# Performance work log

Hardware: AMD Instinct MI355X
Metric: run time of the kernel (lower is better)

Reference implementation:

```python
import jax, jax.numpy as jnp
import numpy as np
from jax import lax

DIM = 192
HEADS = 8


def conv3d(x, w, b, groups=1, pad=0):
    # x: [B,C,T,H,W], w: [O, C//groups, kt, kh, kw]
    out = lax.conv_general_dilated(
        x, w, window_strides=(1, 1, 1),
        padding=[(pad, pad)] * 3,
        dimension_numbers=('NCDHW', 'OIDHW', 'NCDHW'),
        feature_group_count=groups)
    return out + b[None, :, None, None, None]


def setup_inputs() -> dict:
    key = jax.random.key(0)
    ks = jax.random.split(key, 8)
    d = DIM
    x = jax.random.normal(ks[0], (2, d, 8, 64, 64), dtype=jnp.float32)
    qkv_w = jax.random.normal(ks[1], (3 * d, d, 1, 1, 1), dtype=jnp.float32) * 0.02
    qkv_b = jnp.zeros((3 * d,), dtype=jnp.float32)
    dw_w = jax.random.normal(ks[2], (3 * d, 1, 3, 3, 3), dtype=jnp.float32) * 0.02
    dw_b = jnp.zeros((3 * d,), dtype=jnp.float32)
    temperature = jnp.ones((HEADS, 1, 1), dtype=jnp.float32)
    proj_w = jax.random.normal(ks[3], (d, d, 1, 1, 1), dtype=jnp.float32) * 0.02
    proj_b = jnp.zeros((d,), dtype=jnp.float32)
    return {"x": x, "qkv_w": qkv_w, "qkv_b": qkv_b, "dw_w": dw_w,
            "dw_b": dw_b, "temperature": temperature,
            "proj_w": proj_w, "proj_b": proj_b}


def reference(x, qkv_w, qkv_b, dw_w, dw_b, temperature, proj_w, proj_b):
    b, c, t, h, w = x.shape
    head_dim = c // HEADS
    n = t * h * w
    qkv = conv3d(x, qkv_w, qkv_b)                      # [b, 3c, t, h, w]
    qkv = conv3d(qkv, dw_w, dw_b, groups=3 * c, pad=1)  # depthwise 3x3x3
    q, k, v = jnp.split(qkv, 3, axis=1)
    def to_heads(z):
        return z.reshape(b, HEADS, head_dim, n)         # b head c (thw)
    q, k, v = to_heads(q), to_heads(k), to_heads(v)
    # L2 normalize along token axis (F.normalize, eps=1e-12)
    q = q / jnp.maximum(jnp.linalg.norm(q, axis=-1, keepdims=True), 1e-12)
    k = k / jnp.maximum(jnp.linalg.norm(k, axis=-1, keepdims=True), 1e-12)
    attn = jnp.einsum('bhcn,bhdn->bhcd', q, k) * temperature  # [b,H,hd,hd]
    attn = jax.nn.softmax(attn, axis=-1)
    out = jnp.einsum('bhcd,bhdn->bhcn', attn, v)        # [b,H,hd,n]
    out = out.reshape(b, c, t, h, w)
    return conv3d(out, proj_w, proj_b)
```

## Files before the change

kernel.cpp:

```cpp
#include <hip/hip_runtime.h>

#define NTOK 32768
#define CIN 192
#define C3 576
#define HEADS 8
#define HD 24

typedef __attribute__((ext_vector_type(8))) short bf16x8;
typedef __attribute__((ext_vector_type(16))) float f32x16;
typedef __attribute__((ext_vector_type(4))) unsigned int u32x4;

__device__ __forceinline__ float bf2f(unsigned int u) {
  union { unsigned int i; float f; } x; x.i = u << 16; return x.f;
}
__device__ __forceinline__ unsigned short f2bf(float f) {
  union { float f; unsigned int i; } x; x.f = f;
  unsigned int r = x.i + 0x7fffu + ((x.i >> 16) & 1u);
  return (unsigned short)(r >> 16);
}

__global__ __launch_bounds__(256) void k_wfrag(const float* __restrict__ W,
                                               unsigned short* __restrict__ Wf,
                                               int nchunk) {
  const int g = blockIdx.x * 256 + threadIdx.x;
  if (g >= nchunk) return;
  const int ol = g & 63, hi = (g >> 6) & 1, kk = (g >> 7) % 12, ot = g / 1536;
  const float* src = W + (size_t)(ot * 64 + ol) * CIN + kk * 16 + hi * 8;
  bf16x8 p;
#pragma unroll
  for (int e = 0; e < 8; ++e) p[e] = (short)f2bf(src[e]);
  *(bf16x8*)&Wf[(size_t)g * 8] = p;
}

template<int XBF, int OUTF32>
__global__ __launch_bounds__(256, 2) void k_gemm_rr(
    const void* __restrict__ Xv, const unsigned short* __restrict__ Wf0,
    const float* __restrict__ bias, void* __restrict__ Yv, int ot_per,
    long xbs, long ybs, long wbs)
{
  __shared__ __align__(16) unsigned short Xl[192][68];
  const int tid = threadIdx.x;
  const int b = blockIdx.z;
  const int n0 = blockIdx.x * 64;
  const unsigned short* Wf = Wf0 + (size_t)b * wbs;

  if (XBF) {
    const unsigned short* X = (const unsigned short*)Xv + (size_t)b * xbs;
#pragma unroll
    for (int i = 0; i < 12; ++i) {
      const int g = tid + i * 256;
      const int c = g >> 4, nq = (g & 15) * 4;
      *(unsigned long long*)&Xl[c][nq] =
          *(const unsigned long long*)&X[(size_t)c * NTOK + n0 + nq];
    }
  } else {
    const float* X = (const float*)Xv + (size_t)b * xbs;
#pragma unroll
    for (int i = 0; i < 12; ++i) {
      const int g = tid + i * 256;
      const int c = g >> 4, nq = (g & 15) * 4;
      float4 v = *(const float4*)&X[(size_t)c * NTOK + n0 + nq];
      unsigned short p[4] = {f2bf(v.x), f2bf(v.y), f2bf(v.z), f2bf(v.w)};
      *(unsigned long long*)&Xl[c][nq] = *(unsigned long long*)p;
    }
  }
  __syncthreads();

  const int lane = tid & 63;
  const int wv = tid >> 6;
  const int o_w = (wv >> 1) * 32;
  const int n_w = (wv & 1) * 32;
  const int j = lane & 31;
  const int hi = lane >> 5;

  bf16x8 bfr[12];
#pragma unroll
  for (int kk = 0; kk < 12; ++kk)
#pragma unroll
    for (int e = 0; e < 8; ++e)
      bfr[kk][e] = (short)Xl[kk * 16 + hi * 8 + e][n_w + j];

  for (int it = 0; it < ot_per; ++it) {
    const int o0 = it * 64;
    const unsigned short* wp =
        Wf + ((size_t)it * 1536 + hi * 64 + o_w + j) * 8;

    bf16x8 a[12];
#pragma unroll
    for (int kk = 0; kk < 12; ++kk) {
      unsigned long long ad = (unsigned long long)(wp + kk * 1024);
      asm volatile("global_load_dwordx4 %0, %1, off"
                   : "=v"(a[kk]) : "v"(ad));
    }
    asm volatile("s_waitcnt vmcnt(0)" ::: "memory");
    __builtin_amdgcn_sched_barrier(0);

    f32x16 acc0, acc1;
#pragma unroll
    for (int i = 0; i < 16; ++i) { acc0[i] = 0.f; acc1[i] = 0.f; }
#pragma unroll
    for (int kp = 0; kp < 6; ++kp) {
      acc0 = __builtin_amdgcn_mfma_f32_32x32x16_bf16(a[2 * kp], bfr[2 * kp], acc0, 0, 0, 0);
      acc1 = __builtin_amdgcn_mfma_f32_32x32x16_bf16(a[2 * kp + 1], bfr[2 * kp + 1], acc1, 0, 0, 0);
    }

    if (OUTF32) {
      float* Y = (float*)Yv + (size_t)b * ybs;
#pragma unroll
      for (int r = 0; r < 16; ++r) {
        const int row = o_w + (r & 3) + 8 * (r >> 2) + 4 * hi;
        Y[(size_t)(o0 + row) * NTOK + n0 + n_w + j] =
            acc0[r] + acc1[r] + bias[o0 + row];
      }
    } else {
      unsigned short* Y = (unsigned short*)Yv + (size_t)b * ybs;
#pragma unroll
      for (int r = 0; r < 16; ++r) {
        const int row = o_w + (r & 3) + 8 * (r >> 2) + 4 * hi;
        Y[(size_t)(o0 + row) * NTOK + n0 + n_w + j] =
            f2bf(acc0[r] + acc1[r] + bias[o0 + row]);
      }
    }
  }
}

__global__ __launch_bounds__(256, 4) void k_dwconv(
    const unsigned short* __restrict__ in0,
    const float* __restrict__ wdw,
    const float* __restrict__ bdw,
    unsigned short* __restrict__ out0)
{
  __shared__ __align__(16) unsigned short s[8][18][76];
  const int tid = threadIdx.x;
  const int ch = blockIdx.y;
  const int h0 = blockIdx.x * 16;
  const size_t boff = (size_t)blockIdx.z * C3 * NTOK;
  const unsigned short* inch = in0 + boff + (size_t)ch * NTOK;

  for (int r = tid; r < 144; r += 256) {
    const int t = r / 18, rr = r % 18;
    s[t][rr][7] = 0;
    s[t][rr][72] = 0;
  }
  for (int idx = tid; idx < 144 * 8; idx += 256) {
    const int row = idx >> 3, seg = idx & 7;
    const int t = row / 18, rr = row % 18;
    const int h = h0 + rr - 1;
    u32x4 v = {0u, 0u, 0u, 0u};
    if (h >= 0 && h < 64)
      v = *(const u32x4*)&inch[t * 4096 + h * 64 + seg * 8];
    *(u32x4*)&s[t][rr][8 + seg * 8] = v;
  }
  float wr[27];
#pragma unroll
  for (int i = 0; i < 27; ++i) wr[i] = wdw[ch * 27 + i];
  const float bias = bdw[ch];
  __syncthreads();

  const int wloc = tid & 63;
  const int hl0 = (tid >> 6) * 4;
  float acc[8][4];
#pragma unroll
  for (int t = 0; t < 8; ++t)
#pragma unroll
    for (int i = 0; i < 4; ++i) acc[t][i] = 0.f;

#pragma unroll
  for (int tt = 0; tt < 8; ++tt) {
    float v[6][3];
#pragma unroll
    for (int r = 0; r < 6; ++r)
#pragma unroll
      for (int c = 0; c < 3; ++c)
        v[r][c] = bf2f(s[tt][hl0 + r][7 + wloc + c]);
#pragma unroll
    for (int p = 0; p < 3; ++p) {
      const int t = tt + 1 - p;
      if (t < 0 || t > 7) continue;
#pragma unroll
      for (int hi = 0; hi < 4; ++hi) {
        float a = 0.f;
#pragma unroll
        for (int dh = 0; dh < 3; ++dh)
#pragma unroll
          for (int dw = 0; dw < 3; ++dw)
            a += wr[p * 9 + dh * 3 + dw] * v[hi + dh][dw];
        acc[t][hi] += a;
      }
    }
  }

  unsigned short* outch = out0 + boff + (size_t)ch * NTOK;
#pragma unroll
  for (int t = 0; t < 8; ++t)
#pragma unroll
    for (int hi = 0; hi < 4; ++hi)
      outch[t * 4096 + (h0 + hl0 + hi) * 64 + wloc] = f2bf(acc[t][hi] + bias);
}

__global__ __launch_bounds__(256) void k_gram(
    const unsigned short* __restrict__ post0, float* __restrict__ Sp0)
{
  const int tid = threadIdx.x;
  const int h = blockIdx.y;
  const unsigned short* post = post0 + (size_t)blockIdx.z * C3 * NTOK;
  float* Sp = Sp0 + (size_t)blockIdx.z * HEADS * 32 * 640;
  const int lane = tid & 63;
  const int wv = tid >> 6;
  const int c = lane & 31;
  const int off = (lane >> 5) * 8;
  const unsigned short* q = post + (size_t)(h * HD + c) * NTOK;
  const unsigned short* k = post + (size_t)(192 + h * HD + c) * NTOK;

  __shared__ float Sl[24][25];
  __shared__ float nl[48];
  for (int i = tid; i < 600; i += 256) ((float*)Sl)[i] = 0.f;
  if (tid < 48) nl[tid] = 0.f;
  __syncthreads();

  f32x16 acc;
#pragma unroll
  for (int i = 0; i < 16; ++i) acc[i] = 0.f;
  float sqq = 0.f, sqk = 0.f;

  const int base = blockIdx.x * 1024 + wv * 256 + off;
#pragma unroll
  for (int i = 0; i < 16; ++i) {
    const int n = base + i * 16;
    bf16x8 a = *(const bf16x8*)&q[n];
    bf16x8 b = *(const bf16x8*)&k[n];
#pragma unroll
    for (int e = 0; e < 8; ++e) {
      float fa = bf2f((unsigned short)a[e]);
      float fb = bf2f((unsigned short)b[e]);
      sqq += fa * fa;
      sqk += fb * fb;
    }
    acc = __builtin_amdgcn_mfma_f32_32x32x16_bf16(a, b, acc, 0, 0, 0);
  }

  sqq += __shfl_down(sqq, 32, 64);
  sqk += __shfl_down(sqk, 32, 64);
  if (lane < 32 && c < 24) {
    atomicAdd(&nl[c], sqq);
    atomicAdd(&nl[24 + c], sqk);
  }
  if (c < 24) {
#pragma unroll
    for (int r = 0; r < 16; ++r) {
      const int row = (r & 3) + 8 * (r >> 2) + 4 * (lane >> 5);
      if (row < 24) atomicAdd(&Sl[row][c], acc[r]);
    }
  }
  __syncthreads();
  float* outp = Sp + ((size_t)h * 32 + blockIdx.x) * 640;
  for (int i = tid; i < 576; i += 256) outp[i] = Sl[i / 24][i % 24];
  if (tid < 48) outp[576 + tid] = nl[tid];
}

__global__ __launch_bounds__(256) void k_attn_wfrag(
    const float* __restrict__ Sp0, const float* __restrict__ temp,
    const float* __restrict__ projw, unsigned short* __restrict__ wfc0)
{
  const int h = blockIdx.x;
  const int tid = threadIdx.x;
  const float* base = Sp0 + (size_t)blockIdx.y * HEADS * 32 * 640 +
                      (size_t)h * 32 * 640;
  unsigned short* wfc = wfc0 + (size_t)blockIdx.y * 3 * 1536 * 8;

  __shared__ float Ssum[24][25];
  __shared__ float attn[24][25];
  __shared__ float nqs[24], nks[24];

  for (int i = tid; i < 576; i += 256) {
    float a = 0.f;
#pragma unroll 4
    for (int ch = 0; ch < 32; ++ch) a += base[(size_t)ch * 640 + i];
    Ssum[i / 24][i % 24] = a;
  }
  if (tid < 48) {
    float a = 0.f;
#pragma unroll 4
    for (int ch = 0; ch < 32; ++ch) a += base[(size_t)ch * 640 + 576 + tid];
    float nv = fmaxf(sqrtf(a), 1e-12f);
    if (tid < 24) nqs[tid] = nv; else nks[tid - 24] = nv;
  }
  __syncthreads();
  if (tid < 24) {
    const int c = tid;
    const float tmp = temp[h];
    float row[24];
    float m = -1e30f;
#pragma unroll
    for (int d = 0; d < 24; ++d) {
      float v = Ssum[c][d] / (nqs[c] * nks[d]) * tmp;
      row[d] = v;
      m = fmaxf(m, v);
    }
    float ssum = 0.f;
#pragma unroll
    for (int d = 0; d < 24; ++d) { float e = __expf(row[d] - m); row[d] = e; ssum += e; }
    const float inv = 1.f / ssum;
#pragma unroll
    for (int d = 0; d < 24; ++d) attn[c][d] = row[d] * inv;
  }
  __syncthreads();
  for (int e = tid; e < 192 * 24; e += 256) {
    const int o = e / 24, d = e % 24;
    float a = 0.f;
#pragma unroll
    for (int c = 0; c < 24; ++c) a += projw[o * 192 + h * 24 + c] * attn[c][d];
    const int c2 = h * 24 + d;
    const int ot = o >> 6, ol = o & 63;
    const int kk = c2 >> 4, hi = (c2 >> 3) & 1, e2 = c2 & 7;
    wfc[(size_t)((((ot * 12 + kk) * 2 + hi) * 64) + ol) * 8 + e2] = f2bf(a);
  }
}

extern "C" void kernel_launch(void* const* d_in, const int* in_sizes, int n_in,
                              void* d_out, int out_size, void* d_ws, size_t ws_size,
                              hipStream_t stream) {
  const float* x      = (const float*)d_in[0];
  const float* qkv_w  = (const float*)d_in[1];
  const float* qkv_b  = (const float*)d_in[2];
  const float* dw_w   = (const float*)d_in[3];
  const float* dw_b   = (const float*)d_in[4];
  const float* temp   = (const float*)d_in[5];
  const float* proj_w = (const float*)d_in[6];
  const float* proj_b = (const float*)d_in[7];
  float* out = (float*)d_out;

  char* ws = (char*)d_ws;
  size_t off = 0;
  unsigned short* post = (unsigned short*)(ws + off);
  off += (size_t)2 * C3 * NTOK * sizeof(unsigned short);
  unsigned short* pre = (unsigned short*)(ws + off);
  off += (size_t)2 * C3 * NTOK * sizeof(unsigned short);
  float* Sp = (float*)(ws + off);
  off += (size_t)2 * HEADS * 32 * 640 * sizeof(float);
  off = (off + 255) & ~(size_t)255;
  unsigned short* wfq = (unsigned short*)(ws + off);
  off += (size_t)9 * 1536 * 8 * sizeof(unsigned short);
  unsigned short* wfc = (unsigned short*)(ws + off);
  off += (size_t)2 * 3 * 1536 * 8 * sizeof(unsigned short);

  k_wfrag<<<54, 256, 0, stream>>>(qkv_w, wfq, 9 * 1536);

  k_gemm_rr<0, 0><<<dim3(512, 1, 2), 256, 0, stream>>>(
      x, wfq, qkv_b, pre, 9, (long)CIN * NTOK, (long)C3 * NTOK, 0);

  k_dwconv<<<dim3(4, C3, 2), 256, 0, stream>>>(pre, dw_w, dw_b, post);

  k_gram<<<dim3(32, HEADS, 2), 256, 0, stream>>>(post, Sp);

  k_attn_wfrag<<<dim3(HEADS, 2), 256, 0, stream>>>(Sp, temp, proj_w, wfc);

  k_gemm_rr<1, 1><<<dim3(512, 1, 2), 256, 0, stream>>>(
      post + (size_t)384 * NTOK, wfc, proj_b, out, 3,
      (long)C3 * NTOK, (long)CIN * NTOK, (long)3 * 1536 * 8);
}
```

Measured before the change: 146.2 us.

## Split GEMM output tiles across grid y and double-buffer weight fragment loads

The 1x1x1 conv GEMMs now spread output-channel tiles over a second grid dimension (3 chunks), so each block handles 3 or 1 tiles instead of 9 or 3. This raises parallelism, at the cost of each block reloading and re-converting its X tile into LDS. For the QKV GEMM, the weight fragment loads for the next tile are issued before the current tile's MFMAs, using partial vmcnt waits to overlap global loads with compute. The output projection uses one tile per block with no prefetch.

New measurement: 156.0 us. +6.7%, slower.

```diff
diff --git a/kernel.cpp b/kernel.cpp
--- a/kernel.cpp
+++ b/kernel.cpp
@@ -32,15 +32,25 @@
   *(bf16x8*)&Wf[(size_t)g * 8] = p;
 }
 
-template<int XBF, int OUTF32>
+__device__ __forceinline__ void issue12(bf16x8 (&a)[12],
+                                        const unsigned short* p) {
+#pragma unroll
+  for (int kk = 0; kk < 12; ++kk) {
+    unsigned long long ad = (unsigned long long)(p + kk * 1024);
+    asm volatile("global_load_dwordx4 %0, %1, off" : "=v"(a[kk]) : "v"(ad));
+  }
+}
+
+template<int XBF, int OUTF32, int OT>
 __global__ __launch_bounds__(256, 2) void k_gemm_rr(
     const void* __restrict__ Xv, const unsigned short* __restrict__ Wf0,
-    const float* __restrict__ bias, void* __restrict__ Yv, int ot_per,
+    const float* __restrict__ bias, void* __restrict__ Yv,
     long xbs, long ybs, long wbs)
 {
   __shared__ __align__(16) unsigned short Xl[192][68];
   const int tid = threadIdx.x;
   const int b = blockIdx.z;
+  const int oc = blockIdx.y;
   const int n0 = blockIdx.x * 64;
   const unsigned short* Wf = Wf0 + (size_t)b * wbs;
 
@@ -80,21 +90,11 @@
     for (int e = 0; e < 8; ++e)
       bfr[kk][e] = (short)Xl[kk * 16 + hi * 8 + e][n_w + j];
 
-  for (int it = 0; it < ot_per; ++it) {
-    const int o0 = it * 64;
-    const unsigned short* wp =
-        Wf + ((size_t)it * 1536 + hi * 64 + o_w + j) * 8;
-
-    bf16x8 a[12];
-#pragma unroll
-    for (int kk = 0; kk < 12; ++kk) {
-      unsigned long long ad = (unsigned long long)(wp + kk * 1024);
-      asm volatile("global_load_dwordx4 %0, %1, off"
-                   : "=v"(a[kk]) : "v"(ad));
-    }
-    asm volatile("s_waitcnt vmcnt(0)" ::: "memory");
-    __builtin_amdgcn_sched_barrier(0);
-
+  const int ob = oc * OT * 64;
+  const unsigned short* wbase =
+      Wf + ((size_t)(oc * OT) * 1536 + hi * 64 + o_w + j) * 8;
+
+  auto tile = [&](bf16x8 (&a)[12], int o0) {
     f32x16 acc0, acc1;
 #pragma unroll
     for (int i = 0; i < 16; ++i) { acc0[i] = 0.f; acc1[i] = 0.f; }
@@ -103,7 +103,6 @@
       acc0 = __builtin_amdgcn_mfma_f32_32x32x16_bf16(a[2 * kp], bfr[2 * kp], acc0, 0, 0, 0);
       acc1 = __builtin_amdgcn_mfma_f32_32x32x16_bf16(a[2 * kp + 1], bfr[2 * kp + 1], acc1, 0, 0, 0);
     }
-
     if (OUTF32) {
       float* Y = (float*)Yv + (size_t)b * ybs;
 #pragma unroll
@@ -121,6 +120,27 @@
             f2bf(acc0[r] + acc1[r] + bias[o0 + row]);
       }
     }
+  };
+
+  bf16x8 aA[12], aB[12];
+  if (OT == 1) {
+    issue12(aA, wbase);
+    asm volatile("s_waitcnt vmcnt(0)" ::: "memory");
+    __builtin_amdgcn_sched_barrier(0);
+    tile(aA, ob);
+  } else {
+    issue12(aA, wbase);
+    asm volatile("s_waitcnt vmcnt(0)" ::: "memory");
+    __builtin_amdgcn_sched_barrier(0);
+    issue12(aB, wbase + 12288);
+    tile(aA, ob);
+    asm volatile("s_waitcnt vmcnt(16)" ::: "memory");
+    __builtin_amdgcn_sched_barrier(0);
+    issue12(aA, wbase + 24576);
+    tile(aB, ob + 64);
+    asm volatile("s_waitcnt vmcnt(16)" ::: "memory");
+    __builtin_amdgcn_sched_barrier(0);
+    tile(aA, ob + 128);
   }
 }
 
@@ -346,8 +366,8 @@
 
   k_wfrag<<<54, 256, 0, stream>>>(qkv_w, wfq, 9 * 1536);
 
-  k_gemm_rr<0, 0><<<dim3(512, 1, 2), 256, 0, stream>>>(
-      x, wfq, qkv_b, pre, 9, (long)CIN * NTOK, (long)C3 * NTOK, 0);
+  k_gemm_rr<0, 0, 3><<<dim3(512, 3, 2), 256, 0, stream>>>(
+      x, wfq, qkv_b, pre, (long)CIN * NTOK, (long)C3 * NTOK, 0);
 
   k_dwconv<<<dim3(4, C3, 2), 256, 0, stream>>>(pre, dw_w, dw_b, post);
 
@@ -355,7 +375,7 @@
 
   k_attn_wfrag<<<dim3(HEADS, 2), 256, 0, stream>>>(Sp, temp, proj_w, wfc);
 
-  k_gemm_rr<1, 1><<<dim3(512, 1, 2), 256, 0, stream>>>(
-      post + (size_t)384 * NTOK, wfc, proj_b, out, 3,
+  k_gemm_rr<1, 1, 1><<<dim3(512, 3, 2), 256, 0, stream>>>(
+      post + (size_t)384 * NTOK, wfc, proj_b, out,
       (long)C3 * NTOK, (long)CIN * NTOK, (long)3 * 1536 * 8);
 }
```

## Double-buffer weight fragment loads and store X in MFMA fragment layout

Applied to the files above, without the earlier changes.

The 1x1-conv GEMM now prefetches the next output tile's weight fragments into a second register set while MFMAs and stores run for the current tile. It waits with a partial vmcnt instead of draining all loads each iteration. The X tile in shared memory is laid out in 8-element fragment chunks, with rotated scatter writes to spread bank conflicts, so each B fragment is a single 16-byte LDS read instead of eight scalar reads. The depthwise conv kernel's launch bounds drop from 4 to 2 waves per SIMD, which trades occupancy for more registers. The extra register buffer raises register pressure in the GEMM.

Result: slower. 153.6 us (+5.1%).

```diff
diff --git a/kernel.cpp b/kernel.cpp
--- a/kernel.cpp
+++ b/kernel.cpp
@@ -32,17 +32,27 @@
   *(bf16x8*)&Wf[(size_t)g * 8] = p;
 }
 
+__device__ __forceinline__ void issue12(bf16x8 (&a)[12],
+                                        const unsigned short* p) {
+#pragma unroll
+  for (int kk = 0; kk < 12; ++kk) {
+    unsigned long long ad = (unsigned long long)(p + kk * 1024);
+    asm volatile("global_load_dwordx4 %0, %1, off" : "=v"(a[kk]) : "v"(ad));
+  }
+}
+
 template<int XBF, int OUTF32>
 __global__ __launch_bounds__(256, 2) void k_gemm_rr(
     const void* __restrict__ Xv, const unsigned short* __restrict__ Wf0,
     const float* __restrict__ bias, void* __restrict__ Yv, int ot_per,
     long xbs, long ybs, long wbs)
 {
-  __shared__ __align__(16) unsigned short Xl[192][68];
+  __shared__ __align__(16) unsigned short Xf[12 * 128 * 8];
   const int tid = threadIdx.x;
   const int b = blockIdx.z;
   const int n0 = blockIdx.x * 64;
   const unsigned short* Wf = Wf0 + (size_t)b * wbs;
+  const int lsub = tid & 15;
 
   if (XBF) {
     const unsigned short* X = (const unsigned short*)Xv + (size_t)b * xbs;
@@ -50,8 +60,16 @@
     for (int i = 0; i < 12; ++i) {
       const int g = tid + i * 256;
       const int c = g >> 4, nq = (g & 15) * 4;
-      *(unsigned long long*)&Xl[c][nq] =
+      unsigned short t4[4];
+      *(unsigned long long*)t4 =
           *(const unsigned long long*)&X[(size_t)c * NTOK + n0 + nq];
+      const int chunk = (c >> 4) * 128 + ((c >> 3) & 1) * 64 + nq;
+      const int e = c & 7;
+#pragma unroll
+      for (int s = 0; s < 4; ++s) {
+        const int le = (s + lsub) & 3;
+        Xf[(chunk + le) * 8 + e] = t4[le];
+      }
     }
   } else {
     const float* X = (const float*)Xv + (size_t)b * xbs;
@@ -60,8 +78,14 @@
       const int g = tid + i * 256;
       const int c = g >> 4, nq = (g & 15) * 4;
       float4 v = *(const float4*)&X[(size_t)c * NTOK + n0 + nq];
-      unsigned short p[4] = {f2bf(v.x), f2bf(v.y), f2bf(v.z), f2bf(v.w)};
-      *(unsigned long long*)&Xl[c][nq] = *(unsigned long long*)p;
+      float vv[4] = {v.x, v.y, v.z, v.w};
+      const int chunk = (c >> 4) * 128 + ((c >> 3) & 1) * 64 + nq;
+      const int e = c & 7;
+#pragma unroll
+      for (int s = 0; s < 4; ++s) {
+        const int le = (s + lsub) & 3;
+        Xf[(chunk + le) * 8 + e] = f2bf(vv[le]);
+      }
     }
   }
   __syncthreads();
@@ -76,25 +100,11 @@
   bf16x8 bfr[12];
 #pragma unroll
   for (int kk = 0; kk < 12; ++kk)
-#pragma unroll
-    for (int e = 0; e < 8; ++e)
-      bfr[kk][e] = (short)Xl[kk * 16 + hi * 8 + e][n_w + j];
-
-  for (int it = 0; it < ot_per; ++it) {
-    const int o0 = it * 64;
-    const unsigned short* wp =
-        Wf + ((size_t)it * 1536 + hi * 64 + o_w + j) * 8;
-
-    bf16x8 a[12];
-#pragma unroll
-    for (int kk = 0; kk < 12; ++kk) {
-      unsigned long long ad = (unsigned long long)(wp + kk * 1024);
-      asm volatile("global_load_dwordx4 %0, %1, off"
-                   : "=v"(a[kk]) : "v"(ad));
-    }
-    asm volatile("s_waitcnt vmcnt(0)" ::: "memory");
-    __builtin_amdgcn_sched_barrier(0);
-
+    bfr[kk] = *(const bf16x8*)&Xf[(kk * 128 + hi * 64 + n_w + j) * 8];
+
+  const unsigned short* wbase = Wf + ((size_t)hi * 64 + o_w + j) * 8;
+
+  auto tile = [&](bf16x8 (&a)[12], int o0) {
     f32x16 acc0, acc1;
 #pragma unroll
     for (int i = 0; i < 16; ++i) { acc0[i] = 0.f; acc1[i] = 0.f; }
@@ -103,7 +113,6 @@
       acc0 = __builtin_amdgcn_mfma_f32_32x32x16_bf16(a[2 * kp], bfr[2 * kp], acc0, 0, 0, 0);
       acc1 = __builtin_amdgcn_mfma_f32_32x32x16_bf16(a[2 * kp + 1], bfr[2 * kp + 1], acc1, 0, 0, 0);
     }
-
     if (OUTF32) {
       float* Y = (float*)Yv + (size_t)b * ybs;
 #pragma unroll
@@ -121,10 +130,31 @@
             f2bf(acc0[r] + acc1[r] + bias[o0 + row]);
       }
     }
-  }
-}
-
-__global__ __launch_bounds__(256, 4) void k_dwconv(
+  };
+
+  bf16x8 aA[12], aB[12];
+  issue12(aA, wbase);
+  asm volatile("s_waitcnt vmcnt(0)" ::: "memory");
+  __builtin_amdgcn_sched_barrier(0);
+
+  int it = 0;
+  while (true) {
+    if (it + 1 < ot_per) issue12(aB, wbase + (size_t)(it + 1) * 12288);
+    tile(aA, it * 64);
+    if (it + 1 >= ot_per) break;
+    asm volatile("s_waitcnt vmcnt(16)" ::: "memory");
+    __builtin_amdgcn_sched_barrier(0);
+    ++it;
+    if (it + 1 < ot_per) issue12(aA, wbase + (size_t)(it + 1) * 12288);
+    tile(aB, it * 64);
+    if (it + 1 >= ot_per) break;
+    asm volatile("s_waitcnt vmcnt(16)" ::: "memory");
+    __builtin_amdgcn_sched_barrier(0);
+    ++it;
+  }
+}
+
+__global__ __launch_bounds__(256, 2) void k_dwconv(
     const unsigned short* __restrict__ in0,
     const float* __restrict__ wdw,
     const float* __restrict__ bdw,
```
